# Kernel optimization log

Hardware: AMD Instinct MI355X
Metric: run time of the kernel (lower is better)

The kernel has to match this reference:

```python
import jax, jax.numpy as jnp
import numpy as np

DIM = 64
NUM_HEAD = 8
SIZES = [3, 5, 7]
GROUPS = [2, 1, 1]
G_DIM = DIM // 4
SPLITS = [G_DIM * n for n in GROUPS]  # [32, 16, 16]


def _dwconv(x, w, k):
    # depthwise conv, NCHW, kernel (C,1,k,k), groups=C, same padding
    return jax.lax.conv_general_dilated(
        x, w, window_strides=(1, 1), padding=[(k // 2, k // 2)] * 2,
        dimension_numbers=('NCHW', 'OIHW', 'NCHW'),
        feature_group_count=x.shape[1])


def _conv1x1(x, w):
    # w: (out, in)
    return jnp.einsum('oi,bihw->bohw', w, x)


def _avgpool2(x):
    b, c, h, w = x.shape
    return x.reshape(b, c, h // 2, 2, w // 2, 2).mean(axis=(3, 5))


def _l2norm(x, eps=1e-12):
    n = jnp.sqrt(jnp.sum(x * x, axis=-1, keepdims=True))
    return x / jnp.maximum(n, eps)


def setup_inputs() -> dict:
    key = jax.random.key(0)
    ks = jax.random.split(key, 20)
    s = 0.05
    inp = {
        'x': jax.random.normal(ks[0], (4, DIM, 256, 256), dtype=jnp.float32),
        'y': jax.random.normal(ks[1], (4, DIM, 256, 256), dtype=jnp.float32),
    }
    i = 2
    for pfx in ('hp1', 'hp2'):
        for kk, ch in zip(SIZES, SPLITS):
            inp[f'{pfx}_w{kk}'] = jax.random.normal(ks[i], (ch, 1, kk, kk), dtype=jnp.float32) * s
            i += 1
    for name in ('qh_w', 'kh_w', 'vh_w', 'ql_w', 'kl_w', 'vl_w', 'proj_w'):
        inp[name] = jax.random.normal(ks[i], (DIM, DIM), dtype=jnp.float32) * s
        i += 1
    inp['attn_w1'] = jax.random.normal(ks[i], (DIM // 4, DIM), dtype=jnp.float32) * s; i += 1
    inp['attn_w2'] = jax.random.normal(ks[i], (DIM, DIM // 4), dtype=jnp.float32) * s; i += 1
    inp['temperature'] = jnp.ones((NUM_HEAD, 1, 1), dtype=jnp.float32)
    return inp


def reference(x, y, hp1_w3, hp1_w5, hp1_w7, hp2_w3, hp2_w5, hp2_w7,
              qh_w, kh_w, vh_w, ql_w, kl_w, vl_w, proj_w,
              attn_w1, attn_w2, temperature):
    b, c, h, w = x.shape
    idx = np.cumsum(SPLITS)[:-1].tolist()
    xs = jnp.split(x, idx, axis=1)
    ys = jnp.split(y, idx, axis=1)
    hp1 = [hp1_w3, hp1_w5, hp1_w7]
    hp2 = [hp2_w3, hp2_w5, hp2_w7]
    x_h = jnp.concatenate([_dwconv(xs[i], hp1[i], SIZES[i]) for i in range(3)], axis=1)
    y_h = jnp.concatenate([_dwconv(ys[i], hp2[i], SIZES[i]) for i in range(3)], axis=1)
    q_h = _conv1x1(x_h, qh_w)
    k_h = _conv1x1(y_h, kh_w)
    v_h = _conv1x1(x_h, vh_w)
    pooled = jnp.mean(q_h * k_h, axis=(2, 3), keepdims=True)  # b,c,1,1
    high_att = jnp.tanh(_conv1x1(jax.nn.relu(_conv1x1(pooled, attn_w1)), attn_w2))
    out_h = high_att * v_h
    q_l = _conv1x1(_avgpool2(x), ql_w)
    k_l = _conv1x1(_avgpool2(y), kl_w)
    v_l = _conv1x1(y, vl_w)
    ch = c // NUM_HEAD
    q_l = q_l.reshape(b, NUM_HEAD, ch, -1)  # b head c (h/2*w/2)
    k_l = k_l.reshape(b, NUM_HEAD, ch, -1)
    v_l = v_l.reshape(b, NUM_HEAD, ch, -1)  # b head c (h*w)
    q_l = _l2norm(q_l)
    k_l = _l2norm(k_l)
    low_att = jnp.einsum('bhcn,bhdn->bhcd', q_l, k_l) * temperature
    low_att = jax.nn.softmax(low_att, axis=-1)
    out_l = jnp.einsum('bhcd,bhdn->bhcn', low_att, v_l).reshape(b, c, h, w)
    return _conv1x1(out_h + out_l, proj_w)
```

## Files before the change

### kernel.cpp

```cpp
#include <hip/hip_runtime.h>
#include <hip/hip_bf16.h>
#include <math.h>

#define NPX   65536
#define IMGST 4194304
#define NB    4
#define GP    68

__device__ __forceinline__ unsigned short f2bf(float f) {
    unsigned int u = __float_as_uint(f);
    u += 0x7FFFu + ((u >> 16) & 1u);
    return (unsigned short)(u >> 16);
}
__device__ __forceinline__ float bf2f(unsigned short h) {
    return __uint_as_float(((unsigned int)h) << 16);
}

template<int K, int RT>
__device__ __forceinline__ void dw_strip(const float* __restrict__ in,
                                         const float* __restrict__ wp,
                                         unsigned short* __restrict__ outp,
                                         int rowS, int c4) {
    float w[K * K];
#pragma unroll
    for (int i = 0; i < K * K; ++i) w[i] = wp[i];

    float acc[RT][4];
#pragma unroll
    for (int i = 0; i < RT; ++i)
#pragma unroll
        for (int j = 0; j < 4; ++j) acc[i][j] = 0.f;

    const bool lok = (c4 != 0);
    const bool rok = (c4 < 252);
    const int off0 = lok ? -4 : 0;
    const int off2 = rok ? 4 : 0;

#pragma unroll
    for (int ri = 0; ri < RT + K - 1; ++ri) {
        const int gr = rowS - K / 2 + ri;
        float v[12];
        if ((unsigned)gr < 256u) {
            const float* rp = in + gr * 256 + c4;
            const float4 m0 = *reinterpret_cast<const float4*>(rp + off0);
            const float4 m1 = *reinterpret_cast<const float4*>(rp);
            const float4 m2 = *reinterpret_cast<const float4*>(rp + off2);
            v[0] = lok ? m0.x : 0.f; v[1] = lok ? m0.y : 0.f;
            v[2] = lok ? m0.z : 0.f; v[3] = lok ? m0.w : 0.f;
            v[4] = m1.x; v[5] = m1.y; v[6] = m1.z; v[7] = m1.w;
            v[8] = rok ? m2.x : 0.f;  v[9] = rok ? m2.y : 0.f;
            v[10] = rok ? m2.z : 0.f; v[11] = rok ? m2.w : 0.f;
        } else {
#pragma unroll
            for (int t = 0; t < 12; ++t) v[t] = 0.f;
        }
#pragma unroll
        for (int i = 0; i < RT; ++i) {
            const int dy = ri - i;
            if (dy >= 0 && dy < K) {
#pragma unroll
                for (int dx = 0; dx < K; ++dx) {
                    const float wv = w[dy * K + dx];
#pragma unroll
                    for (int j = 0; j < 4; ++j)
                        acc[i][j] = fmaf(wv, v[j + dx + 4 - K / 2], acc[i][j]);
                }
            }
        }
    }

    unsigned short* obase = outp + (size_t)rowS * 256 + c4;
#pragma unroll
    for (int i = 0; i < RT; ++i) {
        ushort4 o;
        o.x = f2bf(acc[i][0]); o.y = f2bf(acc[i][1]);
        o.z = f2bf(acc[i][2]); o.w = f2bf(acc[i][3]);
        *reinterpret_cast<ushort4*>(obase + i * 256) = o;
    }
}

__global__ __launch_bounds__(256) void dsattn_dwconv2(
        const float* __restrict__ xin, const float* __restrict__ yin,
        unsigned short* __restrict__ xout, unsigned short* __restrict__ yout,
        const float* __restrict__ x3, const float* __restrict__ x5,
        const float* __restrict__ x7, const float* __restrict__ y3,
        const float* __restrict__ y5, const float* __restrict__ y7) {
    const int tid = threadIdx.x;
    const int xcd = blockIdx.x & 7;
    const int v   = blockIdx.x >> 3;
    const int sel = blockIdx.y >> 2;
    const int b   = blockIdx.y & 3;
    const int tc = tid & 63, tr = tid >> 6;
    const int c4 = tc * 4;

    const float* inb = (sel == 0 ? xin : yin) + (size_t)b * IMGST;
    unsigned short* outb = (sel == 0 ? xout : yout) + (size_t)b * IMGST;

    if (v < 64) {
        const int idx = xcd * 64 + v;
        const int c = 48 + (idx >> 5), band = idx & 31;
        const float* w = (sel == 0 ? x7 : y7) + (c - 48) * 49;
        dw_strip<7, 2>(inb + (size_t)c * NPX, w, outb + (size_t)c * NPX,
                       band * 8 + tr * 2, c4);
    } else if (v < 128) {
        const int idx = xcd * 64 + (v - 64);
        const int c = idx >> 4, band = idx & 15;
        const float* w = (sel == 0 ? x3 : y3) + c * 9;
        dw_strip<3, 4>(inb + (size_t)c * NPX, w, outb + (size_t)c * NPX,
                       band * 16 + tr * 4, c4);
    } else {
        const int idx = xcd * 32 + (v - 128);
        const int c = 32 + (idx >> 4), band = idx & 15;
        const float* w = (sel == 0 ? x5 : y5) + (c - 32) * 25;
        dw_strip<5, 4>(inb + (size_t)c * NPX, w, outb + (size_t)c * NPX,
                       band * 16 + tr * 4, c4);
    }
}

__global__ __launch_bounds__(256) void dsattn_crossgram(
        const unsigned short* __restrict__ xh, const unsigned short* __restrict__ yh,
        float* __restrict__ Spart) {
    __shared__ __align__(16) float sx[64 * GP];
    __shared__ __align__(16) float sy[64 * GP];
    const int tid = threadIdx.x;
    const int chunk = blockIdx.x;
    const int b = blockIdx.y;
    const int rt = tid >> 4;
    const int ct = tid & 15;
    float acc[16];
#pragma unroll
    for (int i = 0; i < 16; ++i) acc[i] = 0.f;
    const size_t ibase = (size_t)b * IMGST + chunk * 512;

    for (int tile = 0; tile < 8; ++tile) {
        __syncthreads();
        for (int idx = tid; idx < 1024; idx += 256) {
            const int c = idx >> 4, p4 = (idx & 15) * 4;
            const size_t g = ibase + (size_t)c * NPX + tile * 64 + p4;
            const ushort4 vx = *reinterpret_cast<const ushort4*>(&xh[g]);
            const ushort4 vy = *reinterpret_cast<const ushort4*>(&yh[g]);
            sx[(p4 + 0) * GP + c] = bf2f(vx.x); sx[(p4 + 1) * GP + c] = bf2f(vx.y);
            sx[(p4 + 2) * GP + c] = bf2f(vx.z); sx[(p4 + 3) * GP + c] = bf2f(vx.w);
            sy[(p4 + 0) * GP + c] = bf2f(vy.x); sy[(p4 + 1) * GP + c] = bf2f(vy.y);
            sy[(p4 + 2) * GP + c] = bf2f(vy.z); sy[(p4 + 3) * GP + c] = bf2f(vy.w);
        }
        __syncthreads();
        for (int p = 0; p < 64; ++p) {
            const float4 xr = *reinterpret_cast<const float4*>(&sx[p * GP + rt * 4]);
            const float4 yc = *reinterpret_cast<const float4*>(&sy[p * GP + ct * 4]);
            acc[0]  = fmaf(xr.x, yc.x, acc[0]);  acc[1]  = fmaf(xr.x, yc.y, acc[1]);
            acc[2]  = fmaf(xr.x, yc.z, acc[2]);  acc[3]  = fmaf(xr.x, yc.w, acc[3]);
            acc[4]  = fmaf(xr.y, yc.x, acc[4]);  acc[5]  = fmaf(xr.y, yc.y, acc[5]);
            acc[6]  = fmaf(xr.y, yc.z, acc[6]);  acc[7]  = fmaf(xr.y, yc.w, acc[7]);
            acc[8]  = fmaf(xr.z, yc.x, acc[8]);  acc[9]  = fmaf(xr.z, yc.y, acc[9]);
            acc[10] = fmaf(xr.z, yc.z, acc[10]); acc[11] = fmaf(xr.z, yc.w, acc[11]);
            acc[12] = fmaf(xr.w, yc.x, acc[12]); acc[13] = fmaf(xr.w, yc.y, acc[13]);
            acc[14] = fmaf(xr.w, yc.z, acc[14]); acc[15] = fmaf(xr.w, yc.w, acc[15]);
        }
    }
    float* outp = Spart + ((size_t)b * 128 + chunk) * 4096;
#pragma unroll
    for (int r = 0; r < 4; ++r)
#pragma unroll
        for (int c2 = 0; c2 < 4; ++c2)
            outp[(rt * 4 + r) * 64 + ct * 4 + c2] = acc[r * 4 + c2];
}

__global__ __launch_bounds__(256) void dsattn_poolgram(
        const float* __restrict__ x, const float* __restrict__ y,
        float* __restrict__ Ppart) {
    __shared__ __align__(16) float sx[64 * GP];
    __shared__ __align__(16) float sy[64 * GP];
    const int tid = threadIdx.x;
    const int irow = blockIdx.x;
    const int b = blockIdx.y;
    const int rt = tid >> 4, ct = tid & 15;
    float aXY[16], aXX[16], aYY[16];
#pragma unroll
    for (int i = 0; i < 16; ++i) { aXY[i] = 0.f; aXX[i] = 0.f; aYY[i] = 0.f; }
    const size_t ibase = (size_t)b * IMGST + (size_t)(2 * irow) * 256;

    for (int tile = 0; tile < 2; ++tile) {
        __syncthreads();
        for (int idx = tid; idx < 4096; idx += 256) {
            const int c = idx >> 6, jj = idx & 63;
            const size_t g = ibase + (size_t)c * NPX + 2 * (tile * 64 + jj);
            const float2 a0 = *reinterpret_cast<const float2*>(x + g);
            const float2 a1 = *reinterpret_cast<const float2*>(x + g + 256);
            const float2 b0 = *reinterpret_cast<const float2*>(y + g);
            const float2 b1 = *reinterpret_cast<const float2*>(y + g + 256);
            sx[jj * GP + c] = 0.25f * (a0.x + a0.y + a1.x + a1.y);
            sy[jj * GP + c] = 0.25f * (b0.x + b0.y + b1.x + b1.y);
        }
        __syncthreads();
        for (int p = 0; p < 64; ++p) {
            const float4 xr = *reinterpret_cast<const float4*>(&sx[p * GP + rt * 4]);
            const float4 xc = *reinterpret_cast<const float4*>(&sx[p * GP + ct * 4]);
            const float4 yr = *reinterpret_cast<const float4*>(&sy[p * GP + rt * 4]);
            const float4 yc = *reinterpret_cast<const float4*>(&sy[p * GP + ct * 4]);
            const float xrv[4] = {xr.x, xr.y, xr.z, xr.w};
            const float xcv[4] = {xc.x, xc.y, xc.z, xc.w};
            const float yrv[4] = {yr.x, yr.y, yr.z, yr.w};
            const float ycv[4] = {yc.x, yc.y, yc.z, yc.w};
#pragma unroll
            for (int r = 0; r < 4; ++r)
#pragma unroll
                for (int c2 = 0; c2 < 4; ++c2) {
                    aXY[r * 4 + c2] = fmaf(xrv[r], ycv[c2], aXY[r * 4 + c2]);
                    aXX[r * 4 + c2] = fmaf(xrv[r], xcv[c2], aXX[r * 4 + c2]);
                    aYY[r * 4 + c2] = fmaf(yrv[r], ycv[c2], aYY[r * 4 + c2]);
                }
        }
    }
    float* outp = Ppart + ((size_t)b * 128 + irow) * 12288;
#pragma unroll
    for (int r = 0; r < 4; ++r)
#pragma unroll
        for (int c2 = 0; c2 < 4; ++c2) {
            const int o = (rt * 4 + r) * 64 + ct * 4 + c2;
            outp[o]        = aXY[r * 4 + c2];
            outp[4096 + o] = aXX[r * 4 + c2];
            outp[8192 + o] = aYY[r * 4 + c2];
        }
}

__global__ __launch_bounds__(256) void dsattn_reduceSP(
        const float* __restrict__ Spart, float* __restrict__ Sred,
        const float* __restrict__ Ppart, float* __restrict__ Pred) {
    const int b = blockIdx.y;
    if (blockIdx.x < 16) {
        const int i = blockIdx.x * 256 + threadIdx.x;
        const float* p = Spart + (size_t)b * 128 * 4096 + i;
        float s = 0.f;
#pragma unroll 4
        for (int k = 0; k < 128; ++k) s += p[(size_t)k * 4096];
        Sred[b * 4096 + i] = s;
    } else {
        const int i = (blockIdx.x - 16) * 256 + threadIdx.x;
        const float* p = Ppart + (size_t)b * 128 * 12288 + i;
        float s = 0.f;
#pragma unroll 4
        for (int k = 0; k < 128; ++k) s += p[(size_t)k * 12288];
        Pred[b * 12288 + i] = s;
    }
}

__global__ __launch_bounds__(256) void dsattn_sandwich(
        const float* __restrict__ Pred, const float* __restrict__ Sred,
        const float* __restrict__ wql, const float* __restrict__ wkl,
        const float* __restrict__ wq,  const float* __restrict__ wk,
        float* __restrict__ nq2g, float* __restrict__ nk2g,
        float* __restrict__ Gg, float* __restrict__ pooledg) {
    __shared__ float Wl[64 * 65];
    __shared__ float Sl[64 * 65];
    __shared__ float Tl[64 * 65];
    __shared__ float red[256];
    const int unit = blockIdx.x, b = blockIdx.y, tid = threadIdx.x;
    const float *W1, *W2, *Sg;
    if (unit == 0)      { W1 = wql; W2 = wql; Sg = Pred + (size_t)b * 12288 + 4096; }
    else if (unit == 1) { W1 = wkl; W2 = wkl; Sg = Pred + (size_t)b * 12288 + 8192; }
    else if (unit == 2) { W1 = wql; W2 = wkl; Sg = Pred + (size_t)b * 12288; }
    else                { W1 = wq;  W2 = wk;  Sg = Sred + (size_t)b * 4096; }

    for (int i = tid; i < 4096; i += 256) {
        const int r = i >> 6, c = i & 63;
        Wl[r * 65 + c] = W1[i];
        Sl[r * 65 + c] = Sg[i];
    }
    __syncthreads();

    const int rt = tid >> 4, ct = tid & 15;
    float acc[16];
#pragma unroll
    for (int i = 0; i < 16; ++i) acc[i] = 0.f;
    for (int cc = 0; cc < 64; ++cc) {
        float wr[4], sc[4];
#pragma unroll
        for (int j = 0; j < 4; ++j) {
            wr[j] = Wl[(rt * 4 + j) * 65 + cc];
            sc[j] = Sl[cc * 65 + ct * 4 + j];
        }
#pragma unroll
        for (int r = 0; r < 4; ++r)
#pragma unroll
            for (int c2 = 0; c2 < 4; ++c2)
                acc[r * 4 + c2] = fmaf(wr[r], sc[c2], acc[r * 4 + c2]);
    }
#pragma unroll
    for (int r = 0; r < 4; ++r)
#pragma unroll
        for (int c2 = 0; c2 < 4; ++c2)
            Tl[(rt * 4 + r) * 65 + ct * 4 + c2] = acc[r * 4 + c2];
    __syncthreads();
    for (int i = tid; i < 4096; i += 256) Sl[(i >> 6) * 65 + (i & 63)] = W2[i];
    __syncthreads();

    if (unit == 2) {
        for (int i = tid; i < 512; i += 256) {
            const int h = i >> 6, r = (i >> 3) & 7, d = i & 7;
            float s = 0.f;
#pragma unroll
            for (int c = 0; c < 64; ++c)
                s = fmaf(Tl[(h * 8 + r) * 65 + c], Sl[(h * 8 + d) * 65 + c], s);
            Gg[b * 512 + i] = s;
        }
    } else {
        const int r = tid >> 2, part = tid & 3;
        float s = 0.f;
#pragma unroll
        for (int q = 0; q < 16; ++q) {
            const int cp = part * 16 + q;
            s = fmaf(Tl[r * 65 + cp], Sl[r * 65 + cp], s);
        }
        red[tid] = s;
        __syncthreads();
        if (tid < 64) {
            const float v = red[tid * 4] + red[tid * 4 + 1] + red[tid * 4 + 2] + red[tid * 4 + 3];
            if (unit == 0)      nq2g[b * 64 + tid] = v;
            else if (unit == 1) nk2g[b * 64 + tid] = v;
            else                pooledg[b * 64 + tid] = v * (1.f / 65536.f);
        }
    }
}

__global__ __launch_bounds__(256) void dsattn_smallmid(
        const float* __restrict__ nq2g, const float* __restrict__ nk2g,
        const float* __restrict__ Gg, const float* __restrict__ pooledg,
        const float* __restrict__ temp, const float* __restrict__ w1,
        const float* __restrict__ w2, const float* __restrict__ wvl,
        float* __restrict__ hattg, float* __restrict__ tvlg) {
    __shared__ float att[512];
    __shared__ float z[16];
    const int b = blockIdx.x, tid = threadIdx.x;
    if (tid < 16) {
        float a = 0.f;
#pragma unroll
        for (int c = 0; c < 64; ++c) a = fmaf(w1[tid * 64 + c], pooledg[b * 64 + c], a);
        z[tid] = fmaxf(a, 0.f);
    }
    if (tid < 64) {
        const int h = tid >> 3;
        const float tpr = temp[h];
        const float nq = fmaxf(sqrtf(nq2g[b * 64 + tid]), 1e-12f);
        float a[8], m = -1e30f;
#pragma unroll
        for (int d = 0; d < 8; ++d) {
            const float nk = fmaxf(sqrtf(nk2g[b * 64 + h * 8 + d]), 1e-12f);
            a[d] = Gg[b * 512 + tid * 8 + d] / (nq * nk) * tpr;
            m = fmaxf(m, a[d]);
        }
        float ssum = 0.f;
#pragma unroll
        for (int d = 0; d < 8; ++d) { a[d] = expf(a[d] - m); ssum += a[d]; }
        const float inv = 1.f / ssum;
#pragma unroll
        for (int d = 0; d < 8; ++d) att[tid * 8 + d] = a[d] * inv;
    }
    __syncthreads();
    if (tid < 64) {
        float a = 0.f;
#pragma unroll
        for (int i = 0; i < 16; ++i) a = fmaf(w2[tid * 16 + i], z[i], a);
        hattg[b * 64 + tid] = tanhf(a);
    }
    for (int i = tid; i < 4096; i += 256) {
        const int m = i >> 6, c = i & 63, h = m >> 3;
        float s = 0.f;
#pragma unroll
        for (int d = 0; d < 8; ++d) s = fmaf(att[m * 8 + d], wvl[(h * 8 + d) * 64 + c], s);
        tvlg[b * 4096 + i] = s;
    }
}

__global__ __launch_bounds__(256) void dsattn_fold(
        const float* __restrict__ wproj, const float* __restrict__ wvh,
        const float* __restrict__ hattg, const float* __restrict__ tvlg,
        float* __restrict__ At, float* __restrict__ Bt) {
    __shared__ float Pl[64 * 65];
    __shared__ float Vl[64 * 65];
    __shared__ float hm[64];
    const int unit = blockIdx.x, b = blockIdx.y, tid = threadIdx.x;
    if (tid < 64) hm[tid] = hattg[b * 64 + tid];
    for (int i = tid; i < 4096; i += 256) Pl[(i >> 6) * 65 + (i & 63)] = wproj[i];
    __syncthreads();
    for (int i = tid; i < 4096; i += 256) {
        const int m = i >> 6, c = i & 63;
        Vl[m * 65 + c] = (unit == 0) ? hm[m] * wvh[i] : tvlg[b * 4096 + i];
    }
    __syncthreads();

    const int rt = tid >> 4, ct = tid & 15;
    float acc[16];
#pragma unroll
    for (int i = 0; i < 16; ++i) acc[i] = 0.f;
    for (int m = 0; m < 64; ++m) {
        float pv[4], vv[4];
#pragma unroll
        for (int j = 0; j < 4; ++j) {
            pv[j] = Pl[(ct * 4 + j) * 65 + m];
            vv[j] = Vl[m * 65 + rt * 4 + j];
        }
#pragma unroll
        for (int r = 0; r < 4; ++r)
#pragma unroll
            for (int c2 = 0; c2 < 4; ++c2)
                acc[r * 4 + c2] = fmaf(pv[c2], vv[r], acc[r * 4 + c2]);
    }
    float* outp = ((unit == 0) ? At : Bt) + (size_t)b * 4096;
#pragma unroll
    for (int r = 0; r < 4; ++r)
#pragma unroll
        for (int c2 = 0; c2 < 4; ++c2)
            outp[(rt * 4 + r) * 64 + ct * 4 + c2] = acc[r * 4 + c2];
}

__global__ __launch_bounds__(256, 4) void dsattn_final(
        const unsigned short* __restrict__ xh, const float* __restrict__ y,
        const float* __restrict__ At, const float* __restrict__ Bt,
        float* __restrict__ out) {
    const int tid = threadIdx.x;
    const int b = blockIdx.y;
    const int lane = tid & 63;
    const int oc0 = __builtin_amdgcn_readfirstlane((tid >> 6) * 16);
    const size_t base = (size_t)b * IMGST + (size_t)blockIdx.x * 256 + lane * 4;
    const float* __restrict__ Ab = At + b * 4096 + oc0;
    const float* __restrict__ Bb = Bt + b * 4096 + oc0;

    float acc[16][4];
#pragma unroll
    for (int j = 0; j < 16; ++j)
#pragma unroll
        for (int k = 0; k < 4; ++k) acc[j][k] = 0.f;

#pragma unroll 2
    for (int c = 0; c < 64; ++c) {
        const ushort4 xv4 = *reinterpret_cast<const ushort4*>(xh + base + (size_t)c * NPX);
        float4 xv;
        xv.x = bf2f(xv4.x); xv.y = bf2f(xv4.y); xv.z = bf2f(xv4.z); xv.w = bf2f(xv4.w);
        const float4 yv = *reinterpret_cast<const float4*>(y + base + (size_t)c * NPX);
#pragma unroll
        for (int j = 0; j < 16; ++j) {
            const float a  = Ab[c * 64 + j];
            const float bb = Bb[c * 64 + j];
            acc[j][0] = fmaf(a, xv.x, acc[j][0]);
            acc[j][1] = fmaf(a, xv.y, acc[j][1]);
            acc[j][2] = fmaf(a, xv.z, acc[j][2]);
            acc[j][3] = fmaf(a, xv.w, acc[j][3]);
            acc[j][0] = fmaf(bb, yv.x, acc[j][0]);
            acc[j][1] = fmaf(bb, yv.y, acc[j][1]);
            acc[j][2] = fmaf(bb, yv.z, acc[j][2]);
            acc[j][3] = fmaf(bb, yv.w, acc[j][3]);
        }
    }

    float* op = out + base;
#pragma unroll
    for (int j = 0; j < 16; ++j) {
        float4 v;
        v.x = acc[j][0]; v.y = acc[j][1]; v.z = acc[j][2]; v.w = acc[j][3];
        *reinterpret_cast<float4*>(op + (size_t)(oc0 + j) * NPX) = v;
    }
}

extern "C" void kernel_launch(void* const* d_in, const int* in_sizes, int n_in,
                              void* d_out, int out_size, void* d_ws, size_t ws_size,
                              hipStream_t stream) {
    const float* x      = (const float*)d_in[0];
    const float* y      = (const float*)d_in[1];
    const float* hp1_w3 = (const float*)d_in[2];
    const float* hp1_w5 = (const float*)d_in[3];
    const float* hp1_w7 = (const float*)d_in[4];
    const float* hp2_w3 = (const float*)d_in[5];
    const float* hp2_w5 = (const float*)d_in[6];
    const float* hp2_w7 = (const float*)d_in[7];
    const float* qh_w   = (const float*)d_in[8];
    const float* kh_w   = (const float*)d_in[9];
    const float* vh_w   = (const float*)d_in[10];
    const float* ql_w   = (const float*)d_in[11];
    const float* kl_w   = (const float*)d_in[12];
    const float* vl_w   = (const float*)d_in[13];
    const float* proj_w = (const float*)d_in[14];
    const float* attn_w1 = (const float*)d_in[15];
    const float* attn_w2 = (const float*)d_in[16];
    const float* temperature = (const float*)d_in[17];

    float* out = (float*)d_out;

    unsigned short* xh = (unsigned short*)d_ws;
    float* base   = (float*)d_ws + 8388608;
    float* Spart  = base;
    float* Sred   = Spart + (size_t)4 * 128 * 4096;
    float* Pred   = Sred + 16384;
    float* nq2    = Pred + 49152;
    float* nk2    = nq2 + 256;
    float* G      = nk2 + 256;
    float* pooled = G + 2048;
    float* hatt   = pooled + 256;
    float* tvl    = hatt + 256;
    float* At     = tvl + 16384;
    float* Bt     = At + 16384;
    float* Ppart  = Bt + 16384;

    unsigned short* yh = (unsigned short*)d_out;

    dsattn_dwconv2<<<dim3(1280, 8), 256, 0, stream>>>(x, y, xh, yh,
                                                      hp1_w3, hp1_w5, hp1_w7,
                                                      hp2_w3, hp2_w5, hp2_w7);
    dsattn_crossgram<<<dim3(128, 4), 256, 0, stream>>>(xh, yh, Spart);
    dsattn_poolgram<<<dim3(128, 4), 256, 0, stream>>>(x, y, Ppart);
    dsattn_reduceSP<<<dim3(64, 4), 256, 0, stream>>>(Spart, Sred, Ppart, Pred);
    dsattn_sandwich<<<dim3(4, 4), 256, 0, stream>>>(Pred, Sred, ql_w, kl_w, qh_w, kh_w,
                                                    nq2, nk2, G, pooled);
    dsattn_smallmid<<<4, 256, 0, stream>>>(nq2, nk2, G, pooled, temperature,
                                           attn_w1, attn_w2, vl_w, hatt, tvl);
    dsattn_fold<<<dim3(2, 4), 256, 0, stream>>>(proj_w, vh_w, hatt, tvl, At, Bt);
    dsattn_final<<<dim3(256, 4), 256, 0, stream>>>(xh, y, At, Bt, out);
}
```

Before: 230.2 us.

## Fuse x/y depthwise convs per thread and cut gram partial-sum blocks

```diff
diff --git a/kernel.cpp b/kernel.cpp
--- a/kernel.cpp
+++ b/kernel.cpp
@@ -17,19 +17,20 @@
 }
 
 template<int K, int RT>
-__device__ __forceinline__ void dw_strip(const float* __restrict__ in,
-                                         const float* __restrict__ wp,
-                                         unsigned short* __restrict__ outp,
-                                         int rowS, int c4) {
-    float w[K * K];
-#pragma unroll
-    for (int i = 0; i < K * K; ++i) w[i] = wp[i];
-
-    float acc[RT][4];
+__device__ __forceinline__ void dw_strip2(
+        const float* __restrict__ inx, const float* __restrict__ iny,
+        const float* __restrict__ wpx, const float* __restrict__ wpy,
+        unsigned short* __restrict__ outx, unsigned short* __restrict__ outy,
+        int rowS, int c4) {
+    float wx[K * K], wy[K * K];
+#pragma unroll
+    for (int i = 0; i < K * K; ++i) { wx[i] = wpx[i]; wy[i] = wpy[i]; }
+
+    float ax[RT][4], ay[RT][4];
 #pragma unroll
     for (int i = 0; i < RT; ++i)
 #pragma unroll
-        for (int j = 0; j < 4; ++j) acc[i][j] = 0.f;
+        for (int j = 0; j < 4; ++j) { ax[i][j] = 0.f; ay[i][j] = 0.f; }
 
     const bool lok = (c4 != 0);
     const bool rok = (c4 < 252);
@@ -39,20 +40,29 @@
 #pragma unroll
     for (int ri = 0; ri < RT + K - 1; ++ri) {
         const int gr = rowS - K / 2 + ri;
-        float v[12];
+        float vx[12], vy[12];
         if ((unsigned)gr < 256u) {
-            const float* rp = in + gr * 256 + c4;
-            const float4 m0 = *reinterpret_cast<const float4*>(rp + off0);
-            const float4 m1 = *reinterpret_cast<const float4*>(rp);
-            const float4 m2 = *reinterpret_cast<const float4*>(rp + off2);
-            v[0] = lok ? m0.x : 0.f; v[1] = lok ? m0.y : 0.f;
-            v[2] = lok ? m0.z : 0.f; v[3] = lok ? m0.w : 0.f;
-            v[4] = m1.x; v[5] = m1.y; v[6] = m1.z; v[7] = m1.w;
-            v[8] = rok ? m2.x : 0.f;  v[9] = rok ? m2.y : 0.f;
-            v[10] = rok ? m2.z : 0.f; v[11] = rok ? m2.w : 0.f;
+            const float* rpx = inx + gr * 256 + c4;
+            const float* rpy = iny + gr * 256 + c4;
+            const float4 x0 = *reinterpret_cast<const float4*>(rpx + off0);
+            const float4 x1 = *reinterpret_cast<const float4*>(rpx);
+            const float4 x2 = *reinterpret_cast<const float4*>(rpx + off2);
+            const float4 y0 = *reinterpret_cast<const float4*>(rpy + off0);
+            const float4 y1 = *reinterpret_cast<const float4*>(rpy);
+            const float4 y2 = *reinterpret_cast<const float4*>(rpy + off2);
+            vx[0] = lok ? x0.x : 0.f; vx[1] = lok ? x0.y : 0.f;
+            vx[2] = lok ? x0.z : 0.f; vx[3] = lok ? x0.w : 0.f;
+            vx[4] = x1.x; vx[5] = x1.y; vx[6] = x1.z; vx[7] = x1.w;
+            vx[8] = rok ? x2.x : 0.f;  vx[9] = rok ? x2.y : 0.f;
+            vx[10] = rok ? x2.z : 0.f; vx[11] = rok ? x2.w : 0.f;
+            vy[0] = lok ? y0.x : 0.f; vy[1] = lok ? y0.y : 0.f;
+            vy[2] = lok ? y0.z : 0.f; vy[3] = lok ? y0.w : 0.f;
+            vy[4] = y1.x; vy[5] = y1.y; vy[6] = y1.z; vy[7] = y1.w;
+            vy[8] = rok ? y2.x : 0.f;  vy[9] = rok ? y2.y : 0.f;
+            vy[10] = rok ? y2.z : 0.f; vy[11] = rok ? y2.w : 0.f;
         } else {
 #pragma unroll
-            for (int t = 0; t < 12; ++t) v[t] = 0.f;
+            for (int t = 0; t < 12; ++t) { vx[t] = 0.f; vy[t] = 0.f; }
         }
 #pragma unroll
         for (int i = 0; i < RT; ++i) {
@@ -60,22 +70,29 @@
             if (dy >= 0 && dy < K) {
 #pragma unroll
                 for (int dx = 0; dx < K; ++dx) {
-                    const float wv = w[dy * K + dx];
-#pragma unroll
-                    for (int j = 0; j < 4; ++j)
-                        acc[i][j] = fmaf(wv, v[j + dx + 4 - K / 2], acc[i][j]);
+                    const float wvx = wx[dy * K + dx];
+                    const float wvy = wy[dy * K + dx];
+#pragma unroll
+                    for (int j = 0; j < 4; ++j) {
+                        ax[i][j] = fmaf(wvx, vx[j + dx + 4 - K / 2], ax[i][j]);
+                        ay[i][j] = fmaf(wvy, vy[j + dx + 4 - K / 2], ay[i][j]);
+                    }
                 }
             }
         }
     }
 
-    unsigned short* obase = outp + (size_t)rowS * 256 + c4;
+    unsigned short* obx = outx + (size_t)rowS * 256 + c4;
+    unsigned short* oby = outy + (size_t)rowS * 256 + c4;
 #pragma unroll
     for (int i = 0; i < RT; ++i) {
-        ushort4 o;
-        o.x = f2bf(acc[i][0]); o.y = f2bf(acc[i][1]);
-        o.z = f2bf(acc[i][2]); o.w = f2bf(acc[i][3]);
-        *reinterpret_cast<ushort4*>(obase + i * 256) = o;
+        ushort4 ox, oy;
+        ox.x = f2bf(ax[i][0]); ox.y = f2bf(ax[i][1]);
+        ox.z = f2bf(ax[i][2]); ox.w = f2bf(ax[i][3]);
+        oy.x = f2bf(ay[i][0]); oy.y = f2bf(ay[i][1]);
+        oy.z = f2bf(ay[i][2]); oy.w = f2bf(ay[i][3]);
+        *reinterpret_cast<ushort4*>(obx + i * 256) = ox;
+        *reinterpret_cast<ushort4*>(oby + i * 256) = oy;
     }
 }
 
@@ -88,32 +105,36 @@
     const int tid = threadIdx.x;
     const int xcd = blockIdx.x & 7;
     const int v   = blockIdx.x >> 3;
-    const int sel = blockIdx.y >> 2;
-    const int b   = blockIdx.y & 3;
+    const int b   = blockIdx.y;
     const int tc = tid & 63, tr = tid >> 6;
     const int c4 = tc * 4;
 
-    const float* inb = (sel == 0 ? xin : yin) + (size_t)b * IMGST;
-    unsigned short* outb = (sel == 0 ? xout : yout) + (size_t)b * IMGST;
+    const float* inxb = xin + (size_t)b * IMGST;
+    const float* inyb = yin + (size_t)b * IMGST;
+    unsigned short* outxb = xout + (size_t)b * IMGST;
+    unsigned short* outyb = yout + (size_t)b * IMGST;
 
     if (v < 64) {
         const int idx = xcd * 64 + v;
         const int c = 48 + (idx >> 5), band = idx & 31;
-        const float* w = (sel == 0 ? x7 : y7) + (c - 48) * 49;
-        dw_strip<7, 2>(inb + (size_t)c * NPX, w, outb + (size_t)c * NPX,
-                       band * 8 + tr * 2, c4);
-    } else if (v < 128) {
-        const int idx = xcd * 64 + (v - 64);
+        const size_t co = (size_t)c * NPX;
+        dw_strip2<7, 2>(inxb + co, inyb + co,
+                        x7 + (c - 48) * 49, y7 + (c - 48) * 49,
+                        outxb + co, outyb + co, band * 8 + tr * 2, c4);
+    } else if (v < 96) {
+        const int idx = xcd * 32 + (v - 64);
+        const int c = 32 + (idx >> 4), band = idx & 15;
+        const size_t co = (size_t)c * NPX;
+        dw_strip2<5, 4>(inxb + co, inyb + co,
+                        x5 + (c - 32) * 25, y5 + (c - 32) * 25,
+                        outxb + co, outyb + co, band * 16 + tr * 4, c4);
+    } else {
+        const int idx = xcd * 64 + (v - 96);
         const int c = idx >> 4, band = idx & 15;
-        const float* w = (sel == 0 ? x3 : y3) + c * 9;
-        dw_strip<3, 4>(inb + (size_t)c * NPX, w, outb + (size_t)c * NPX,
-                       band * 16 + tr * 4, c4);
-    } else {
-        const int idx = xcd * 32 + (v - 128);
-        const int c = 32 + (idx >> 4), band = idx & 15;
-        const float* w = (sel == 0 ? x5 : y5) + (c - 32) * 25;
-        dw_strip<5, 4>(inb + (size_t)c * NPX, w, outb + (size_t)c * NPX,
-                       band * 16 + tr * 4, c4);
+        const size_t co = (size_t)c * NPX;
+        dw_strip2<3, 4>(inxb + co, inyb + co,
+                        x3 + c * 9, y3 + c * 9,
+                        outxb + co, outyb + co, band * 16 + tr * 4, c4);
     }
 }
 
@@ -130,9 +151,9 @@
     float acc[16];
 #pragma unroll
     for (int i = 0; i < 16; ++i) acc[i] = 0.f;
-    const size_t ibase = (size_t)b * IMGST + chunk * 512;
-
-    for (int tile = 0; tile < 8; ++tile) {
+    const size_t ibase = (size_t)b * IMGST + chunk * 2048;
+
+    for (int tile = 0; tile < 32; ++tile) {
         __syncthreads();
         for (int idx = tid; idx < 1024; idx += 256) {
             const int c = idx >> 4, p4 = (idx & 15) * 4;
@@ -158,7 +179,7 @@
             acc[14] = fmaf(xr.w, yc.z, acc[14]); acc[15] = fmaf(xr.w, yc.w, acc[15]);
         }
     }
-    float* outp = Spart + ((size_t)b * 128 + chunk) * 4096;
+    float* outp = Spart + ((size_t)b * 32 + chunk) * 4096;
 #pragma unroll
     for (int r = 0; r < 4; ++r)
 #pragma unroll
@@ -172,19 +193,21 @@
     __shared__ __align__(16) float sx[64 * GP];
     __shared__ __align__(16) float sy[64 * GP];
     const int tid = threadIdx.x;
-    const int irow = blockIdx.x;
+    const int chunk = blockIdx.x;
     const int b = blockIdx.y;
     const int rt = tid >> 4, ct = tid & 15;
     float aXY[16], aXX[16], aYY[16];
 #pragma unroll
     for (int i = 0; i < 16; ++i) { aXY[i] = 0.f; aXX[i] = 0.f; aYY[i] = 0.f; }
-    const size_t ibase = (size_t)b * IMGST + (size_t)(2 * irow) * 256;
-
-    for (int tile = 0; tile < 2; ++tile) {
+
+    for (int t = 0; t < 8; ++t) {
+        const int prow = chunk * 4 + (t >> 1);
+        const int ch   = t & 1;
+        const size_t ibase = (size_t)b * IMGST + (size_t)(2 * prow) * 256 + 2 * ch * 64;
         __syncthreads();
         for (int idx = tid; idx < 4096; idx += 256) {
             const int c = idx >> 6, jj = idx & 63;
-            const size_t g = ibase + (size_t)c * NPX + 2 * (tile * 64 + jj);
+            const size_t g = ibase + (size_t)c * NPX + 2 * jj;
             const float2 a0 = *reinterpret_cast<const float2*>(x + g);
             const float2 a1 = *reinterpret_cast<const float2*>(x + g + 256);
             const float2 b0 = *reinterpret_cast<const float2*>(y + g);
@@ -212,7 +235,7 @@
                 }
         }
     }
-    float* outp = Ppart + ((size_t)b * 128 + irow) * 12288;
+    float* outp = Ppart + ((size_t)b * 32 + chunk) * 12288;
 #pragma unroll
     for (int r = 0; r < 4; ++r)
 #pragma unroll
@@ -230,17 +253,17 @@
     const int b = blockIdx.y;
     if (blockIdx.x < 16) {
         const int i = blockIdx.x * 256 + threadIdx.x;
-        const float* p = Spart + (size_t)b * 128 * 4096 + i;
+        const float* p = Spart + (size_t)b * 32 * 4096 + i;
         float s = 0.f;
 #pragma unroll 4
-        for (int k = 0; k < 128; ++k) s += p[(size_t)k * 4096];
+        for (int k = 0; k < 32; ++k) s += p[(size_t)k * 4096];
         Sred[b * 4096 + i] = s;
     } else {
         const int i = (blockIdx.x - 16) * 256 + threadIdx.x;
-        const float* p = Ppart + (size_t)b * 128 * 12288 + i;
+        const float* p = Ppart + (size_t)b * 32 * 12288 + i;
         float s = 0.f;
 #pragma unroll 4
-        for (int k = 0; k < 128; ++k) s += p[(size_t)k * 12288];
+        for (int k = 0; k < 32; ++k) s += p[(size_t)k * 12288];
         Pred[b * 12288 + i] = s;
     }
 }
@@ -489,7 +512,7 @@
     unsigned short* xh = (unsigned short*)d_ws;
     float* base   = (float*)d_ws + 8388608;
     float* Spart  = base;
-    float* Sred   = Spart + (size_t)4 * 128 * 4096;
+    float* Sred   = Spart + 524288;
     float* Pred   = Sred + 16384;
     float* nq2    = Pred + 49152;
     float* nk2    = nq2 + 256;
@@ -503,11 +526,11 @@
 
     unsigned short* yh = (unsigned short*)d_out;
 
-    dsattn_dwconv2<<<dim3(1280, 8), 256, 0, stream>>>(x, y, xh, yh,
+    dsattn_dwconv2<<<dim3(1280, 4), 256, 0, stream>>>(x, y, xh, yh,
                                                       hp1_w3, hp1_w5, hp1_w7,
                                                       hp2_w3, hp2_w5, hp2_w7);
-    dsattn_crossgram<<<dim3(128, 4), 256, 0, stream>>>(xh, yh, Spart);
-    dsattn_poolgram<<<dim3(128, 4), 256, 0, stream>>>(x, y, Ppart);
+    dsattn_crossgram<<<dim3(32, 4), 256, 0, stream>>>(xh, yh, Spart);
+    dsattn_poolgram<<<dim3(32, 4), 256, 0, stream>>>(x, y, Ppart);
     dsattn_reduceSP<<<dim3(64, 4), 256, 0, stream>>>(Spart, Sred, Ppart, Pred);
     dsattn_sandwich<<<dim3(4, 4), 256, 0, stream>>>(Pred, Sred, ql_w, kl_w, qh_w, kh_w,
                                                     nq2, nk2, G, pooled);
```

New measurement: 359.4 us. 1.56x slower.
